# Performance work log

Hardware: AMD Instinct MI355X
Metric: run time of the kernel (lower is better)

The kernel has to match this reference:

```python
import jax, jax.numpy as jnp
import numpy as np

N_NODES = 2708  # hardcoded dim_size in the original aggregate()
IN_C = 2048
OUT_C = 512
N_EDGES = 500000


def setup_inputs() -> dict:
    key = jax.random.key(0)
    k1, k2, k3, k4 = jax.random.split(key, 4)
    x = jax.random.normal(k1, (N_NODES, IN_C), dtype=jnp.float32)
    edge_index = jax.random.randint(k2, (2, N_EDGES), 0, N_NODES, dtype=jnp.int32)
    weight = jax.random.normal(k3, (OUT_C, IN_C), dtype=jnp.float32) * (1.0 / np.sqrt(IN_C))
    bias = jax.random.normal(k4, (OUT_C,), dtype=jnp.float32) * 0.01
    return {"x": x, "edge_index": edge_index, "weight": weight, "bias": bias}


def reference(x, edge_index, weight, bias):
    # Dropout omitted (eval-mode equivalent; p=0.5 only active in training).
    # F.linear: y = x @ W^T + b  -> [N, OUT_C]
    h = jnp.einsum('ni,oi->no', x, weight) + bias
    # message: gather source-node features per edge  -> [E, OUT_C]
    msgs = h[edge_index[0]]
    # aggregate: scatter_add into destination nodes (fixed dim_size=2708)
    out = jax.ops.segment_sum(msgs, edge_index[1], num_segments=N_NODES)
    return out
```

## Files before the change

kernel.cpp:

```cpp
#include <hip/hip_runtime.h>
#include <stdint.h>

typedef unsigned short u16;
typedef unsigned int u32;

#define N_NODES 2708
#define IN_C    2048
#define OUT_C   512
#define MP      2816
#define KP      2816

using floatx4 = __attribute__((ext_vector_type(4))) float;
using short8  = __attribute__((ext_vector_type(8))) short;

constexpr size_t XB_OFF = 0;
constexpr size_t XB_SZ  = (size_t)MP * IN_C * 2;
constexpr size_t WB_OFF = XB_OFF + XB_SZ;
constexpr size_t WB_SZ  = (size_t)OUT_C * IN_C * 2;
constexpr size_t HT_OFF = WB_OFF + WB_SZ;
constexpr size_t HT_SZ  = (size_t)OUT_C * MP * 2;
constexpr size_t AC_OFF = HT_OFF + HT_SZ;
constexpr size_t AC_SZ  = (size_t)MP * KP * 2;
constexpr size_t P_OFF  = AC_OFF + AC_SZ;
constexpr size_t P_SZ   = (size_t)2 * OUT_C * MP * 4;

static __device__ __forceinline__ u16 f2bf(float f) {
  union { float f; u32 u; } v; v.f = f;
  u32 r = v.u + 0x7fffu + ((v.u >> 16) & 1u);
  return (u16)(r >> 16);
}

constexpr int XBLK = MP * IN_C / 8 / 256;
constexpr int WBLK = OUT_C * IN_C / 8 / 256;
constexpr int ZF4  = (int)(AC_SZ / 16);
constexpr int ZBLK = ZF4 / 256;
constexpr int PREP_BLK = XBLK + WBLK + ZBLK;

__global__ void k_prep(const float* __restrict__ x, const float* __restrict__ w,
                       u16* __restrict__ xb, u16* __restrict__ wb,
                       float4* __restrict__ zac) {
  const int b = blockIdx.x, tid = threadIdx.x;
  if (b < XBLK) {
    const int row = b, col = tid * 8;
    union { u16 u[8]; uint4 v; } o;
    if (row < N_NODES) {
      float4 v0 = *(const float4*)&x[(size_t)row * IN_C + col];
      float4 v1 = *(const float4*)&x[(size_t)row * IN_C + col + 4];
      o.u[0]=f2bf(v0.x); o.u[1]=f2bf(v0.y); o.u[2]=f2bf(v0.z); o.u[3]=f2bf(v0.w);
      o.u[4]=f2bf(v1.x); o.u[5]=f2bf(v1.y); o.u[6]=f2bf(v1.z); o.u[7]=f2bf(v1.w);
    } else {
      o.v = make_uint4(0, 0, 0, 0);
    }
    *(uint4*)&xb[(size_t)row * IN_C + col] = o.v;
  } else if (b < XBLK + WBLK) {
    const int idx = ((b - XBLK) * 256 + tid) * 8;
    float4 v0 = *(const float4*)&w[idx];
    float4 v1 = *(const float4*)&w[idx + 4];
    union { u16 u[8]; uint4 v; } o;
    o.u[0]=f2bf(v0.x); o.u[1]=f2bf(v0.y); o.u[2]=f2bf(v0.z); o.u[3]=f2bf(v0.w);
    o.u[4]=f2bf(v1.x); o.u[5]=f2bf(v1.y); o.u[6]=f2bf(v1.z); o.u[7]=f2bf(v1.w);
    *(uint4*)&wb[idx] = o.v;
  } else {
    const int i = (b - XBLK - WBLK) * 256 + tid;
    zac[i] = make_float4(0.f, 0.f, 0.f, 0.f);
  }
}

__global__ void k_count(const int* __restrict__ ei, u32* __restrict__ Ac, int E) {
  int e = blockIdx.x * 256 + threadIdx.x;
  if (e < E) {
    int src = ei[e];
    int dst = ei[E + e];
    u32 idx = (u32)dst * KP + (u32)src;
    atomicAdd(&Ac[idx >> 1], 1u << ((idx & 1) * 16));
  }
}

static __device__ __forceinline__ u32 cvt2(u32 w) {
  float lo = (float)(w & 0xffffu), hi = (float)(w >> 16);
  return (u32)f2bf(lo) | ((u32)f2bf(hi) << 16);
}
__global__ void k_cvtA(uint4* __restrict__ A, int n) {
  int i = blockIdx.x * 256 + threadIdx.x;
  if (i < n) {
    uint4 v = A[i];
    A[i] = make_uint4(cvt2(v.x), cvt2(v.y), cvt2(v.z), cvt2(v.w));
  }
}

template<int LDK, int NKI, int EPI>
__global__ __launch_bounds__(256, 2) void k_gemm(
    const u16* __restrict__ A, const u16* __restrict__ B, float* __restrict__ dst) {
  __shared__ u16 lA[3][128 * 64];
  __shared__ u16 lB[3][64 * 64];
  const int tid = threadIdx.x, lane = tid & 63, wid = tid >> 6;

  const int cpx = (int)gridDim.x >> 3;
  const int orig = blockIdx.x;
  const int swz = (orig & 7) * cpx + (orig >> 3);
  const int bn = swz & 7;
  const int rest = swz >> 3;
  const int ks = (rest >= 22) ? 1 : 0;
  const int bm = rest - ks * 22;
  const int bmr = bm * 128, bnr = bn * 64;
  const long k0b = (long)ks * LDK;

  const int wr = wid >> 1, wc = wid & 1;

  const int swzl = ((lane & 7) ^ ((lane >> 3) & 7)) * 16;
  const char* ag[4];
  const char* bg[2];
#pragma unroll
  for (int j = 0; j < 4; ++j) {
    int c = wid + 4 * j, row = 8 * c + (lane >> 3);
    ag[j] = (const char*)A + (size_t)(bmr + row) * (LDK * 2) + k0b + swzl;
  }
#pragma unroll
  for (int j = 0; j < 2; ++j) {
    int c = wid + 4 * j, row = 8 * c + (lane >> 3);
    bg[j] = (const char*)B + (size_t)(bnr + row) * (LDK * 2) + k0b + swzl;
  }

#define STAGE(bb, tt) do {                                                        \
  _Pragma("unroll")                                                               \
  for (int j = 0; j < 4; ++j)                                                     \
    __builtin_amdgcn_global_load_lds(                                             \
      (const __attribute__((address_space(1))) u32*)(ag[j] + (size_t)(tt) * 128), \
      (__attribute__((address_space(3))) u32*)&lA[bb][(wid + 4 * j) * 512],       \
      16, 0, 0);                                                                  \
  _Pragma("unroll")                                                               \
  for (int j = 0; j < 2; ++j)                                                     \
    __builtin_amdgcn_global_load_lds(                                             \
      (const __attribute__((address_space(1))) u32*)(bg[j] + (size_t)(tt) * 128), \
      (__attribute__((address_space(3))) u32*)&lB[bb][(wid + 4 * j) * 512],       \
      16, 0, 0);                                                                  \
} while (0)

  floatx4 acc[4][2] = {};

  STAGE(0, 0);
  if (NKI > 1) STAGE(1, 1);
  int cur = 0;
  for (int t = 0; t < NKI; ++t) {
    if (t + 1 < NKI) asm volatile("s_waitcnt vmcnt(6)" ::: "memory");
    else             asm volatile("s_waitcnt vmcnt(0)" ::: "memory");
    __builtin_amdgcn_s_barrier();
    asm volatile("" ::: "memory");
    if (t + 2 < NKI) {
      int nb = cur + 2; if (nb >= 3) nb -= 3;
      STAGE(nb, t + 2);
    }
    const u16* pA = lA[cur];
    const u16* pB = lB[cur];
    short8 af[4][2], bf[2][2];
#pragma unroll
    for (int mi = 0; mi < 4; ++mi)
#pragma unroll
      for (int kk = 0; kk < 2; ++kk) {
        const int row = wr * 64 + mi * 16 + (lane & 15);
        const int col8 = ((kk * 4 + (lane >> 4)) ^ (lane & 7)) * 8;
        af[mi][kk] = *(const short8*)&pA[row * 64 + col8];
      }
#pragma unroll
    for (int ni = 0; ni < 2; ++ni)
#pragma unroll
      for (int kk = 0; kk < 2; ++kk) {
        const int row = wc * 32 + ni * 16 + (lane & 15);
        const int col8 = ((kk * 4 + (lane >> 4)) ^ (lane & 7)) * 8;
        bf[ni][kk] = *(const short8*)&pB[row * 64 + col8];
      }
    __builtin_amdgcn_s_setprio(1);
#pragma unroll
    for (int kk = 0; kk < 2; ++kk)
#pragma unroll
      for (int mi = 0; mi < 4; ++mi)
#pragma unroll
        for (int ni = 0; ni < 2; ++ni)
          acc[mi][ni] = __builtin_amdgcn_mfma_f32_16x16x32_bf16(af[mi][kk], bf[ni][kk], acc[mi][ni], 0, 0, 0);
    __builtin_amdgcn_s_setprio(0);
    ++cur; if (cur >= 3) cur -= 3;
  }
#undef STAGE

  const int lr = (lane >> 4) * 4, lc = lane & 15;
  if (EPI == 0) {
#pragma unroll
    for (int ni = 0; ni < 2; ++ni) {
      const int n = bnr + wc * 32 + ni * 16 + lc;
#pragma unroll
      for (int mi = 0; mi < 4; ++mi) {
        const int m0 = bmr + wr * 64 + mi * 16 + lr;
        *(floatx4*)&dst[((size_t)ks * OUT_C + n) * MP + m0] = acc[mi][ni];
      }
    }
  } else {
#pragma unroll
    for (int mi = 0; mi < 4; ++mi)
#pragma unroll
      for (int j = 0; j < 4; ++j) {
        const int m = bmr + wr * 64 + mi * 16 + lr + j;
#pragma unroll
        for (int ni = 0; ni < 2; ++ni) {
          const int n = bnr + wc * 32 + ni * 16 + lc;
          dst[((size_t)ks * MP + m) * OUT_C + n] = acc[mi][ni][j];
        }
      }
  }
}

__global__ void k_red1(const float* __restrict__ P1, const float* __restrict__ bias,
                       u16* __restrict__ hT) {
  int i8 = blockIdx.x * 256 + threadIdx.x;
  int n = i8 / (MP / 8);
  int m0 = (i8 - n * (MP / 8)) * 8;
  float bv = bias[n];
  const float* p0 = &P1[(size_t)n * MP + m0];
  const float* p1 = p0 + (size_t)OUT_C * MP;
  float4 a0 = *(const float4*)p0, a1 = *(const float4*)(p0 + 4);
  float4 b0 = *(const float4*)p1, b1 = *(const float4*)(p1 + 4);
  union { u16 u[8]; uint4 v; } o;
  o.u[0]=f2bf(a0.x+b0.x+bv); o.u[1]=f2bf(a0.y+b0.y+bv);
  o.u[2]=f2bf(a0.z+b0.z+bv); o.u[3]=f2bf(a0.w+b0.w+bv);
  o.u[4]=f2bf(a1.x+b1.x+bv); o.u[5]=f2bf(a1.y+b1.y+bv);
  o.u[6]=f2bf(a1.z+b1.z+bv); o.u[7]=f2bf(a1.w+b1.w+bv);
  *(uint4*)&hT[(size_t)n * MP + m0] = o.v;
}

__global__ void k_red2(const float* __restrict__ P2, float* __restrict__ out) {
  int i = blockIdx.x * 256 + threadIdx.x;
  size_t o = (size_t)i * 4;
  float4 a = *(const float4*)&P2[o];
  float4 b = *(const float4*)&P2[(size_t)MP * OUT_C + o];
  *(float4*)&out[o] = make_float4(a.x + b.x, a.y + b.y, a.z + b.z, a.w + b.w);
}

extern "C" void kernel_launch(void* const* d_in, const int* in_sizes, int n_in,
                              void* d_out, int out_size, void* d_ws, size_t ws_size,
                              hipStream_t stream) {
  const float* x    = (const float*)d_in[0];
  const int*   ei   = (const int*)d_in[1];
  const float* w    = (const float*)d_in[2];
  const float* bias = (const float*)d_in[3];
  float* out = (float*)d_out;

  char* ws = (char*)d_ws;
  u16*   xb = (u16*)(ws + XB_OFF);
  u16*   wb = (u16*)(ws + WB_OFF);
  u16*   hT = (u16*)(ws + HT_OFF);
  u16*   Ac = (u16*)(ws + AC_OFF);
  float* P  = (float*)(ws + P_OFF);

  const int E = in_sizes[1] / 2;

  k_prep<<<dim3(PREP_BLK), dim3(256), 0, stream>>>(x, w, xb, wb, (float4*)Ac);
  k_count<<<dim3((E + 255) / 256), dim3(256), 0, stream>>>(ei, (u32*)Ac, E);
  k_cvtA<<<dim3(ZF4 / 256), dim3(256), 0, stream>>>((uint4*)Ac, ZF4);
  k_gemm<IN_C, IN_C / 2 / 64, 0><<<dim3(352), dim3(256), 0, stream>>>(xb, wb, P);
  k_red1<<<dim3(OUT_C * MP / 8 / 256), dim3(256), 0, stream>>>(P, bias, hT);
  k_gemm<KP, KP / 2 / 64, 1><<<dim3(352), dim3(256), 0, stream>>>(Ac, hT, P);
  k_red2<<<dim3(N_NODES * OUT_C / 4 / 256), dim3(256), 0, stream>>>(P, out);
}
```

Measured before the change: 147.4 us.

## Fuse all stages into one cooperative persistent kernel with grid syncs

Replaces the seven separate kernel launches with a single cooperative kernel of 512 blocks. The stages (prep, edge counting, convert, GEMM1, reduce1, GEMM2, reduce2) are separated by grid.sync, and the original launch sequence is kept as a fallback if the cooperative launch fails. This aims to remove launch overhead and inter-kernel gaps. In exchange, only 352 blocks do GEMM work while the rest idle, the elementwise phases run as grid-stride loops, and grid barriers add their own cost.

```diff
diff --git a/kernel.cpp b/kernel.cpp
--- a/kernel.cpp
+++ b/kernel.cpp
@@ -1,5 +1,8 @@
 #include <hip/hip_runtime.h>
+#include <hip/hip_cooperative_groups.h>
 #include <stdint.h>
+
+namespace cg = cooperative_groups;
 
 typedef unsigned short u16;
 typedef unsigned int u32;
@@ -24,193 +27,49 @@
 constexpr size_t P_OFF  = AC_OFF + AC_SZ;
 constexpr size_t P_SZ   = (size_t)2 * OUT_C * MP * 4;
 
+constexpr int ZF4 = (int)(AC_SZ / 16);
+constexpr int GEMM_BLK = 352;
+
 static __device__ __forceinline__ u16 f2bf(float f) {
   union { float f; u32 u; } v; v.f = f;
   u32 r = v.u + 0x7fffu + ((v.u >> 16) & 1u);
   return (u16)(r >> 16);
 }
-
-constexpr int XBLK = MP * IN_C / 8 / 256;
-constexpr int WBLK = OUT_C * IN_C / 8 / 256;
-constexpr int ZF4  = (int)(AC_SZ / 16);
-constexpr int ZBLK = ZF4 / 256;
-constexpr int PREP_BLK = XBLK + WBLK + ZBLK;
-
-__global__ void k_prep(const float* __restrict__ x, const float* __restrict__ w,
-                       u16* __restrict__ xb, u16* __restrict__ wb,
-                       float4* __restrict__ zac) {
-  const int b = blockIdx.x, tid = threadIdx.x;
-  if (b < XBLK) {
-    const int row = b, col = tid * 8;
-    union { u16 u[8]; uint4 v; } o;
-    if (row < N_NODES) {
-      float4 v0 = *(const float4*)&x[(size_t)row * IN_C + col];
-      float4 v1 = *(const float4*)&x[(size_t)row * IN_C + col + 4];
-      o.u[0]=f2bf(v0.x); o.u[1]=f2bf(v0.y); o.u[2]=f2bf(v0.z); o.u[3]=f2bf(v0.w);
-      o.u[4]=f2bf(v1.x); o.u[5]=f2bf(v1.y); o.u[6]=f2bf(v1.z); o.u[7]=f2bf(v1.w);
-    } else {
-      o.v = make_uint4(0, 0, 0, 0);
-    }
-    *(uint4*)&xb[(size_t)row * IN_C + col] = o.v;
-  } else if (b < XBLK + WBLK) {
-    const int idx = ((b - XBLK) * 256 + tid) * 8;
-    float4 v0 = *(const float4*)&w[idx];
-    float4 v1 = *(const float4*)&w[idx + 4];
-    union { u16 u[8]; uint4 v; } o;
-    o.u[0]=f2bf(v0.x); o.u[1]=f2bf(v0.y); o.u[2]=f2bf(v0.z); o.u[3]=f2bf(v0.w);
-    o.u[4]=f2bf(v1.x); o.u[5]=f2bf(v1.y); o.u[6]=f2bf(v1.z); o.u[7]=f2bf(v1.w);
-    *(uint4*)&wb[idx] = o.v;
-  } else {
-    const int i = (b - XBLK - WBLK) * 256 + tid;
-    zac[i] = make_float4(0.f, 0.f, 0.f, 0.f);
-  }
-}
-
-__global__ void k_count(const int* __restrict__ ei, u32* __restrict__ Ac, int E) {
-  int e = blockIdx.x * 256 + threadIdx.x;
-  if (e < E) {
-    int src = ei[e];
-    int dst = ei[E + e];
-    u32 idx = (u32)dst * KP + (u32)src;
-    atomicAdd(&Ac[idx >> 1], 1u << ((idx & 1) * 16));
-  }
-}
-
 static __device__ __forceinline__ u32 cvt2(u32 w) {
   float lo = (float)(w & 0xffffu), hi = (float)(w >> 16);
   return (u32)f2bf(lo) | ((u32)f2bf(hi) << 16);
 }
-__global__ void k_cvtA(uint4* __restrict__ A, int n) {
-  int i = blockIdx.x * 256 + threadIdx.x;
-  if (i < n) {
-    uint4 v = A[i];
-    A[i] = make_uint4(cvt2(v.x), cvt2(v.y), cvt2(v.z), cvt2(v.w));
-  }
-}
-
-template<int LDK, int NKI, int EPI>
-__global__ __launch_bounds__(256, 2) void k_gemm(
-    const u16* __restrict__ A, const u16* __restrict__ B, float* __restrict__ dst) {
-  __shared__ u16 lA[3][128 * 64];
-  __shared__ u16 lB[3][64 * 64];
-  const int tid = threadIdx.x, lane = tid & 63, wid = tid >> 6;
-
-  const int cpx = (int)gridDim.x >> 3;
-  const int orig = blockIdx.x;
-  const int swz = (orig & 7) * cpx + (orig >> 3);
-  const int bn = swz & 7;
-  const int rest = swz >> 3;
-  const int ks = (rest >= 22) ? 1 : 0;
-  const int bm = rest - ks * 22;
-  const int bmr = bm * 128, bnr = bn * 64;
-  const long k0b = (long)ks * LDK;
-
-  const int wr = wid >> 1, wc = wid & 1;
-
-  const int swzl = ((lane & 7) ^ ((lane >> 3) & 7)) * 16;
-  const char* ag[4];
-  const char* bg[2];
-#pragma unroll
-  for (int j = 0; j < 4; ++j) {
-    int c = wid + 4 * j, row = 8 * c + (lane >> 3);
-    ag[j] = (const char*)A + (size_t)(bmr + row) * (LDK * 2) + k0b + swzl;
-  }
-#pragma unroll
-  for (int j = 0; j < 2; ++j) {
-    int c = wid + 4 * j, row = 8 * c + (lane >> 3);
-    bg[j] = (const char*)B + (size_t)(bnr + row) * (LDK * 2) + k0b + swzl;
-  }
-
-#define STAGE(bb, tt) do {                                                        \
-  _Pragma("unroll")                                                               \
-  for (int j = 0; j < 4; ++j)                                                     \
-    __builtin_amdgcn_global_load_lds(                                             \
-      (const __attribute__((address_space(1))) u32*)(ag[j] + (size_t)(tt) * 128), \
-      (__attribute__((address_space(3))) u32*)&lA[bb][(wid + 4 * j) * 512],       \
-      16, 0, 0);                                                                  \
-  _Pragma("unroll")                                                               \
-  for (int j = 0; j < 2; ++j)                                                     \
-    __builtin_amdgcn_global_load_lds(                                             \
-      (const __attribute__((address_space(1))) u32*)(bg[j] + (size_t)(tt) * 128), \
-      (__attribute__((address_space(3))) u32*)&lB[bb][(wid + 4 * j) * 512],       \
-      16, 0, 0);                                                                  \
-} while (0)
-
-  floatx4 acc[4][2] = {};
-
-  STAGE(0, 0);
-  if (NKI > 1) STAGE(1, 1);
-  int cur = 0;
-  for (int t = 0; t < NKI; ++t) {
-    if (t + 1 < NKI) asm volatile("s_waitcnt vmcnt(6)" ::: "memory");
-    else             asm volatile("s_waitcnt vmcnt(0)" ::: "memory");
-    __builtin_amdgcn_s_barrier();
-    asm volatile("" ::: "memory");
-    if (t + 2 < NKI) {
-      int nb = cur + 2; if (nb >= 3) nb -= 3;
-      STAGE(nb, t + 2);
-    }
-    const u16* pA = lA[cur];
-    const u16* pB = lB[cur];
-    short8 af[4][2], bf[2][2];
-#pragma unroll
-    for (int mi = 0; mi < 4; ++mi)
-#pragma unroll
-      for (int kk = 0; kk < 2; ++kk) {
-        const int row = wr * 64 + mi * 16 + (lane & 15);
-        const int col8 = ((kk * 4 + (lane >> 4)) ^ (lane & 7)) * 8;
-        af[mi][kk] = *(const short8*)&pA[row * 64 + col8];
-      }
-#pragma unroll
-    for (int ni = 0; ni < 2; ++ni)
-#pragma unroll
-      for (int kk = 0; kk < 2; ++kk) {
-        const int row = wc * 32 + ni * 16 + (lane & 15);
-        const int col8 = ((kk * 4 + (lane >> 4)) ^ (lane & 7)) * 8;
-        bf[ni][kk] = *(const short8*)&pB[row * 64 + col8];
-      }
-    __builtin_amdgcn_s_setprio(1);
-#pragma unroll
-    for (int kk = 0; kk < 2; ++kk)
-#pragma unroll
-      for (int mi = 0; mi < 4; ++mi)
-#pragma unroll
-        for (int ni = 0; ni < 2; ++ni)
-          acc[mi][ni] = __builtin_amdgcn_mfma_f32_16x16x32_bf16(af[mi][kk], bf[ni][kk], acc[mi][ni], 0, 0, 0);
-    __builtin_amdgcn_s_setprio(0);
-    ++cur; if (cur >= 3) cur -= 3;
-  }
-#undef STAGE
-
-  const int lr = (lane >> 4) * 4, lc = lane & 15;
-  if (EPI == 0) {
-#pragma unroll
-    for (int ni = 0; ni < 2; ++ni) {
-      const int n = bnr + wc * 32 + ni * 16 + lc;
-#pragma unroll
-      for (int mi = 0; mi < 4; ++mi) {
-        const int m0 = bmr + wr * 64 + mi * 16 + lr;
-        *(floatx4*)&dst[((size_t)ks * OUT_C + n) * MP + m0] = acc[mi][ni];
-      }
-    }
+
+
+static __device__ __forceinline__ void prep_x_body(int i, const float* __restrict__ x,
+                                                   u16* __restrict__ xb) {
+  const int row = i >> 8, col = (i & 255) * 8;
+  union { u16 u[8]; uint4 v; } o;
+  if (row < N_NODES) {
+    float4 v0 = *(const float4*)&x[(size_t)row * IN_C + col];
+    float4 v1 = *(const float4*)&x[(size_t)row * IN_C + col + 4];
+    o.u[0]=f2bf(v0.x); o.u[1]=f2bf(v0.y); o.u[2]=f2bf(v0.z); o.u[3]=f2bf(v0.w);
+    o.u[4]=f2bf(v1.x); o.u[5]=f2bf(v1.y); o.u[6]=f2bf(v1.z); o.u[7]=f2bf(v1.w);
   } else {
-#pragma unroll
-    for (int mi = 0; mi < 4; ++mi)
-#pragma unroll
-      for (int j = 0; j < 4; ++j) {
-        const int m = bmr + wr * 64 + mi * 16 + lr + j;
-#pragma unroll
-        for (int ni = 0; ni < 2; ++ni) {
-          const int n = bnr + wc * 32 + ni * 16 + lc;
-          dst[((size_t)ks * MP + m) * OUT_C + n] = acc[mi][ni][j];
-        }
-      }
-  }
-}
-
-__global__ void k_red1(const float* __restrict__ P1, const float* __restrict__ bias,
-                       u16* __restrict__ hT) {
-  int i8 = blockIdx.x * 256 + threadIdx.x;
+    o.v = make_uint4(0, 0, 0, 0);
+  }
+  *(uint4*)&xb[(size_t)row * IN_C + col] = o.v;
+}
+
+static __device__ __forceinline__ void prep_w_body(int i, const float* __restrict__ w,
+                                                   u16* __restrict__ wb) {
+  const int idx = i * 8;
+  float4 v0 = *(const float4*)&w[idx];
+  float4 v1 = *(const float4*)&w[idx + 4];
+  union { u16 u[8]; uint4 v; } o;
+  o.u[0]=f2bf(v0.x); o.u[1]=f2bf(v0.y); o.u[2]=f2bf(v0.z); o.u[3]=f2bf(v0.w);
+  o.u[4]=f2bf(v1.x); o.u[5]=f2bf(v1.y); o.u[6]=f2bf(v1.z); o.u[7]=f2bf(v1.w);
+  *(uint4*)&wb[idx] = o.v;
+}
+
+static __device__ __forceinline__ void red1_body(int i8, const float* __restrict__ P1,
+                                                 const float* __restrict__ bias,
+                                                 u16* __restrict__ hT) {
   int n = i8 / (MP / 8);
   int m0 = (i8 - n * (MP / 8)) * 8;
   float bv = bias[n];
@@ -226,12 +85,232 @@
   *(uint4*)&hT[(size_t)n * MP + m0] = o.v;
 }
 
-__global__ void k_red2(const float* __restrict__ P2, float* __restrict__ out) {
-  int i = blockIdx.x * 256 + threadIdx.x;
+static __device__ __forceinline__ void red2_body(int i, const float* __restrict__ P2,
+                                                 float* __restrict__ out) {
   size_t o = (size_t)i * 4;
   float4 a = *(const float4*)&P2[o];
   float4 b = *(const float4*)&P2[(size_t)MP * OUT_C + o];
   *(float4*)&out[o] = make_float4(a.x + b.x, a.y + b.y, a.z + b.z, a.w + b.w);
+}
+
+template<int LDK, int NKI, int EPI>
+static __device__ __forceinline__ void gemm_phase(
+    const u16* __restrict__ A, const u16* __restrict__ B,
+    float* __restrict__ dst, u16* lAp, u16* lBp) {
+  const int tid = threadIdx.x, lane = tid & 63, wid = tid >> 6;
+
+  const int orig = blockIdx.x;
+  const int swz = (orig & 7) * 44 + (orig >> 3);
+  const int bn = swz & 7;
+  const int rest = swz >> 3;
+  const int ks = (rest >= 22) ? 1 : 0;
+  const int bm = rest - ks * 22;
+  const int bmr = bm * 128, bnr = bn * 64;
+  const long k0b = (long)ks * LDK;
+
+  const int wr = wid >> 1, wc = wid & 1;
+
+  const int swzl = ((lane & 7) ^ ((lane >> 3) & 7)) * 16;
+  const char* ag[4];
+  const char* bg[2];
+#pragma unroll
+  for (int j = 0; j < 4; ++j) {
+    int c = wid + 4 * j, row = 8 * c + (lane >> 3);
+    ag[j] = (const char*)A + (size_t)(bmr + row) * (LDK * 2) + k0b + swzl;
+  }
+#pragma unroll
+  for (int j = 0; j < 2; ++j) {
+    int c = wid + 4 * j, row = 8 * c + (lane >> 3);
+    bg[j] = (const char*)B + (size_t)(bnr + row) * (LDK * 2) + k0b + swzl;
+  }
+
+#define STAGE(bb, tt) do {                                                         \
+  _Pragma("unroll")                                                                \
+  for (int j = 0; j < 4; ++j)                                                      \
+    __builtin_amdgcn_global_load_lds(                                              \
+      (const __attribute__((address_space(1))) u32*)(ag[j] + (size_t)(tt) * 128),  \
+      (__attribute__((address_space(3))) u32*)&lAp[(bb) * 8192 + (wid + 4*j)*512], \
+      16, 0, 0);                                                                   \
+  _Pragma("unroll")                                                                \
+  for (int j = 0; j < 2; ++j)                                                      \
+    __builtin_amdgcn_global_load_lds(                                              \
+      (const __attribute__((address_space(1))) u32*)(bg[j] + (size_t)(tt) * 128),  \
+      (__attribute__((address_space(3))) u32*)&lBp[(bb) * 4096 + (wid + 4*j)*512], \
+      16, 0, 0);                                                                   \
+} while (0)
+
+  floatx4 acc[4][2] = {};
+
+  STAGE(0, 0);
+  if (NKI > 1) STAGE(1, 1);
+  int cur = 0;
+  for (int t = 0; t < NKI; ++t) {
+    if (t + 1 < NKI) asm volatile("s_waitcnt vmcnt(6)" ::: "memory");
+    else             asm volatile("s_waitcnt vmcnt(0)" ::: "memory");
+    __builtin_amdgcn_s_barrier();
+    asm volatile("" ::: "memory");
+    if (t + 2 < NKI) {
+      int nb = cur + 2; if (nb >= 3) nb -= 3;
+      STAGE(nb, t + 2);
+    }
+    const u16* pA = lAp + cur * 8192;
+    const u16* pB = lBp + cur * 4096;
+    short8 af[4][2], bf[2][2];
+#pragma unroll
+    for (int mi = 0; mi < 4; ++mi)
+#pragma unroll
+      for (int kk = 0; kk < 2; ++kk) {
+        const int row = wr * 64 + mi * 16 + (lane & 15);
+        const int col8 = ((kk * 4 + (lane >> 4)) ^ (lane & 7)) * 8;
+        af[mi][kk] = *(const short8*)&pA[row * 64 + col8];
+      }
+#pragma unroll
+    for (int ni = 0; ni < 2; ++ni)
+#pragma unroll
+      for (int kk = 0; kk < 2; ++kk) {
+        const int row = wc * 32 + ni * 16 + (lane & 15);
+        const int col8 = ((kk * 4 + (lane >> 4)) ^ (lane & 7)) * 8;
+        bf[ni][kk] = *(const short8*)&pB[row * 64 + col8];
+      }
+    __builtin_amdgcn_s_setprio(1);
+#pragma unroll
+    for (int kk = 0; kk < 2; ++kk)
+#pragma unroll
+      for (int mi = 0; mi < 4; ++mi)
+#pragma unroll
+        for (int ni = 0; ni < 2; ++ni)
+          acc[mi][ni] = __builtin_amdgcn_mfma_f32_16x16x32_bf16(af[mi][kk], bf[ni][kk], acc[mi][ni], 0, 0, 0);
+    __builtin_amdgcn_s_setprio(0);
+    ++cur; if (cur >= 3) cur -= 3;
+  }
+#undef STAGE
+
+  const int lr = (lane >> 4) * 4, lc = lane & 15;
+  if (EPI == 0) {
+#pragma unroll
+    for (int ni = 0; ni < 2; ++ni) {
+      const int n = bnr + wc * 32 + ni * 16 + lc;
+#pragma unroll
+      for (int mi = 0; mi < 4; ++mi) {
+        const int m0 = bmr + wr * 64 + mi * 16 + lr;
+        *(floatx4*)&dst[((size_t)ks * OUT_C + n) * MP + m0] = acc[mi][ni];
+      }
+    }
+  } else {
+#pragma unroll
+    for (int mi = 0; mi < 4; ++mi)
+#pragma unroll
+      for (int j = 0; j < 4; ++j) {
+        const int m = bmr + wr * 64 + mi * 16 + lr + j;
+#pragma unroll
+        for (int ni = 0; ni < 2; ++ni) {
+          const int n = bnr + wc * 32 + ni * 16 + lc;
+          dst[((size_t)ks * MP + m) * OUT_C + n] = acc[mi][ni][j];
+        }
+      }
+  }
+}
+
+__global__ __launch_bounds__(256, 2) void k_mega(
+    const float* __restrict__ x, const int* __restrict__ ei,
+    const float* __restrict__ w, const float* __restrict__ bias,
+    u16* __restrict__ xb, u16* __restrict__ wb, u16* __restrict__ hT,
+    u16* __restrict__ Ac, float* __restrict__ P, float* __restrict__ out,
+    int E) {
+  __shared__ u16 lA[3][128 * 64];
+  __shared__ u16 lB[3][64 * 64];
+  cg::grid_group grid = cg::this_grid();
+  const int gtid = blockIdx.x * 256 + threadIdx.x;
+  const int NT = (int)gridDim.x * 256;
+
+  for (int i = gtid; i < MP * IN_C / 8; i += NT) prep_x_body(i, x, xb);
+  for (int i = gtid; i < OUT_C * IN_C / 8; i += NT) prep_w_body(i, w, wb);
+  {
+    float4* zac = (float4*)Ac;
+    const float4 z = make_float4(0.f, 0.f, 0.f, 0.f);
+    for (int i = gtid; i < ZF4; i += NT) zac[i] = z;
+  }
+  grid.sync();
+  {
+    u32* Ac32 = (u32*)Ac;
+    for (int e = gtid; e < E; e += NT) {
+      int src = ei[e];
+      int dst = ei[E + e];
+      u32 idx = (u32)dst * KP + (u32)src;
+      atomicAdd(&Ac32[idx >> 1], 1u << ((idx & 1) * 16));
+    }
+  }
+  grid.sync();
+  {
+    uint4* A4 = (uint4*)Ac;
+    for (int i = gtid; i < ZF4; i += NT) {
+      uint4 v = A4[i];
+      A4[i] = make_uint4(cvt2(v.x), cvt2(v.y), cvt2(v.z), cvt2(v.w));
+    }
+  }
+  grid.sync();
+  if (blockIdx.x < GEMM_BLK)
+    gemm_phase<IN_C, IN_C / 2 / 64, 0>(xb, wb, P, &lA[0][0], &lB[0][0]);
+  grid.sync();
+  for (int i = gtid; i < OUT_C * MP / 8; i += NT) red1_body(i, P, bias, hT);
+  grid.sync();
+  if (blockIdx.x < GEMM_BLK)
+    gemm_phase<KP, KP / 2 / 64, 1>(Ac, hT, P, &lA[0][0], &lB[0][0]);
+  grid.sync();
+  for (int i = gtid; i < N_NODES * OUT_C / 4; i += NT) red2_body(i, P, out);
+}
+
+constexpr int XBLK = MP * IN_C / 8 / 256;
+constexpr int WBLK = OUT_C * IN_C / 8 / 256;
+constexpr int ZBLK = ZF4 / 256;
+constexpr int PREP_BLK = XBLK + WBLK + ZBLK;
+
+__global__ void k_prep(const float* __restrict__ x, const float* __restrict__ w,
+                       u16* __restrict__ xb, u16* __restrict__ wb,
+                       float4* __restrict__ zac) {
+  const int b = blockIdx.x, tid = threadIdx.x;
+  if (b < XBLK) {
+    prep_x_body(b * 256 + tid, x, xb);
+  } else if (b < XBLK + WBLK) {
+    prep_w_body((b - XBLK) * 256 + tid, w, wb);
+  } else {
+    zac[(b - XBLK - WBLK) * 256 + tid] = make_float4(0.f, 0.f, 0.f, 0.f);
+  }
+}
+
+__global__ void k_count(const int* __restrict__ ei, u32* __restrict__ Ac, int E) {
+  int e = blockIdx.x * 256 + threadIdx.x;
+  if (e < E) {
+    int src = ei[e];
+    int dst = ei[E + e];
+    u32 idx = (u32)dst * KP + (u32)src;
+    atomicAdd(&Ac[idx >> 1], 1u << ((idx & 1) * 16));
+  }
+}
+
+__global__ void k_cvtA(uint4* __restrict__ A, int n) {
+  int i = blockIdx.x * 256 + threadIdx.x;
+  if (i < n) {
+    uint4 v = A[i];
+    A[i] = make_uint4(cvt2(v.x), cvt2(v.y), cvt2(v.z), cvt2(v.w));
+  }
+}
+
+template<int LDK, int NKI, int EPI>
+__global__ __launch_bounds__(256, 2) void k_gemm(
+    const u16* __restrict__ A, const u16* __restrict__ B, float* __restrict__ dst) {
+  __shared__ u16 lA[3][128 * 64];
+  __shared__ u16 lB[3][64 * 64];
+  gemm_phase<LDK, NKI, EPI>(A, B, dst, &lA[0][0], &lB[0][0]);
+}
+
+__global__ void k_red1(const float* __restrict__ P1, const float* __restrict__ bias,
+                       u16* __restrict__ hT) {
+  red1_body(blockIdx.x * 256 + threadIdx.x, P1, bias, hT);
+}
+
+__global__ void k_red2(const float* __restrict__ P2, float* __restrict__ out) {
+  red2_body(blockIdx.x * 256 + threadIdx.x, P2, out);
 }
 
 extern "C" void kernel_launch(void* const* d_in, const int* in_sizes, int n_in,
@@ -250,13 +329,20 @@
   u16*   Ac = (u16*)(ws + AC_OFF);
   float* P  = (float*)(ws + P_OFF);
 
-  const int E = in_sizes[1] / 2;
-
-  k_prep<<<dim3(PREP_BLK), dim3(256), 0, stream>>>(x, w, xb, wb, (float4*)Ac);
-  k_count<<<dim3((E + 255) / 256), dim3(256), 0, stream>>>(ei, (u32*)Ac, E);
-  k_cvtA<<<dim3(ZF4 / 256), dim3(256), 0, stream>>>((uint4*)Ac, ZF4);
-  k_gemm<IN_C, IN_C / 2 / 64, 0><<<dim3(352), dim3(256), 0, stream>>>(xb, wb, P);
-  k_red1<<<dim3(OUT_C * MP / 8 / 256), dim3(256), 0, stream>>>(P, bias, hT);
-  k_gemm<KP, KP / 2 / 64, 1><<<dim3(352), dim3(256), 0, stream>>>(Ac, hT, P);
-  k_red2<<<dim3(N_NODES * OUT_C / 4 / 256), dim3(256), 0, stream>>>(P, out);
-}
+  int E = in_sizes[1] / 2;
+
+  void* args[] = { (void*)&x, (void*)&ei, (void*)&w, (void*)&bias,
+                   (void*)&xb, (void*)&wb, (void*)&hT, (void*)&Ac,
+                   (void*)&P, (void*)&out, (void*)&E };
+  hipError_t rc = hipLaunchCooperativeKernel((const void*)k_mega, dim3(512),
+                                             dim3(256), args, 0, stream);
+  if (rc != hipSuccess) {
+    k_prep<<<dim3(PREP_BLK), dim3(256), 0, stream>>>(x, w, xb, wb, (float4*)Ac);
+    k_count<<<dim3((E + 255) / 256), dim3(256), 0, stream>>>(ei, (u32*)Ac, E);
+    k_cvtA<<<dim3(ZF4 / 256), dim3(256), 0, stream>>>((uint4*)Ac, ZF4);
+    k_gemm<IN_C, IN_C / 2 / 64, 0><<<dim3(GEMM_BLK), dim3(256), 0, stream>>>(xb, wb, P);
+    k_red1<<<dim3(OUT_C * MP / 8 / 256), dim3(256), 0, stream>>>(P, bias, hT);
+    k_gemm<KP, KP / 2 / 64, 1><<<dim3(GEMM_BLK), dim3(256), 0, stream>>>(Ac, hT, P);
+    k_red2<<<dim3(N_NODES * OUT_C / 4 / 256), dim3(256), 0, stream>>>(P, out);
+  }
+}
```

Measured after the change: 510.2 us. 246% more time.
